# Kernel tuning notes

Hardware: AMD Instinct MI355X
Metric: run time of the kernel (lower is better)

Reference implementation:

```python
import jax, jax.numpy as jnp
import numpy as np

E, C, M, H, O = 8, 4096, 1024, 4096, 1024  # experts, capacity, model_dim, hidden, output_dim

def setup_inputs() -> dict:
    key = jax.random.key(0)
    k1, k2, k3, k4, k5 = jax.random.split(key, 5)
    s1 = 1.0 / np.sqrt(M)
    s2 = 1.0 / np.sqrt(H)
    return {
        "x": jax.random.normal(k1, (E, C, M), dtype=jnp.float32),
        "fc1_w": jax.random.normal(k2, (E, M, H), dtype=jnp.float32) * s1,
        "fc1_b": jax.random.normal(k3, (E, H), dtype=jnp.float32) * s1,
        "fc2_w": jax.random.normal(k4, (E, H, O), dtype=jnp.float32) * s2,
        "fc2_b": jax.random.normal(k5, (E, O), dtype=jnp.float32) * s2,
    }

def reference(x, fc1_w, fc1_b, fc2_w, fc2_b):
    # grouped GEMM over experts: [E,C,M] @ [E,M,H] -> [E,C,H]
    y = jnp.einsum('ecm,emh->ech', x, fc1_w) + fc1_b[:, None, :]
    y = jax.nn.relu(y)  # default activation_fn
    # [E,C,H] @ [E,H,O] -> [E,C,O]
    out = jnp.einsum('ech,eho->eco', y, fc2_w) + fc2_b[:, None, :]
    return out
```

## Files before the change

### kernel.cpp

```cpp
#include <hip/hip_runtime.h>
#include <hip/hip_bf16.h>


#define BM 128
#define BN 128
#define BK 32

typedef __attribute__((ext_vector_type(8))) short short8;
typedef __attribute__((ext_vector_type(4))) float f32x4;

typedef const __attribute__((address_space(1))) void GV;
typedef __attribute__((address_space(3))) void LV;

__device__ inline ushort f2bf_rne(float f) {
    union { float f; unsigned u; } v; v.f = f;
    unsigned u = v.u;
    u += 0x7FFFu + ((u >> 16) & 1u);
    return (ushort)(u >> 16);
}

__global__ __launch_bounds__(256) void convert_bf16(
    const float* __restrict__ in, ushort* __restrict__ out, long n) {
    long i = ((long)blockIdx.x * 256 + threadIdx.x) * 8;
    if (i + 7 >= n) return;
    float4 v0 = *(const float4*)&in[i];
    float4 v1 = *(const float4*)&in[i + 4];
    short8 o;
    o[0] = f2bf_rne(v0.x); o[1] = f2bf_rne(v0.y);
    o[2] = f2bf_rne(v0.z); o[3] = f2bf_rne(v0.w);
    o[4] = f2bf_rne(v1.x); o[5] = f2bf_rne(v1.y);
    o[6] = f2bf_rne(v1.z); o[7] = f2bf_rne(v1.w);
    *(short8*)&out[i] = o;
}

__global__ __launch_bounds__(256) void transpose_convert(
    const float* __restrict__ in, ushort* __restrict__ out, int R, int Cn) {
    __shared__ float tile[64][65];
    const int e  = blockIdx.z;
    const float* ine  = in  + (size_t)e * R * Cn;
    ushort*      oute = out + (size_t)e * R * Cn;
    const int r0 = blockIdx.y * 64;
    const int c0 = blockIdx.x * 64;
    const int t  = threadIdx.x;
#pragma unroll
    for (int i = 0; i < 4; ++i) {
        int idx = i * 256 + t;
        int ir  = idx >> 4;
        int icc = (idx & 15) * 4;
        float4 v = *(const float4*)&ine[(size_t)(r0 + ir) * Cn + c0 + icc];
        tile[ir][icc + 0] = v.x; tile[ir][icc + 1] = v.y;
        tile[ir][icc + 2] = v.z; tile[ir][icc + 3] = v.w;
    }
    __syncthreads();
#pragma unroll
    for (int i = 0; i < 2; ++i) {
        int idx = i * 256 + t;
        int ic  = idx >> 3;
        int ir0 = (idx & 7) * 8;
        short8 o;
#pragma unroll
        for (int j = 0; j < 8; ++j) o[j] = f2bf_rne(tile[ir0 + j][ic]);
        *(short8*)&oute[(size_t)(c0 + ic) * R + r0 + ir0] = o;
    }
}

template <bool RELU_BF16_OUT, int GX, int GY, int K, int N>
__global__ __launch_bounds__(256, 2) void gemm_bt(
    const ushort* __restrict__ A, const ushort* __restrict__ Bt,
    const float* __restrict__ bias, void* __restrict__ out) {
    __shared__ ushort As[BM * BK];
    __shared__ ushort Bs[BN * BK];

    constexpr int TOTAL   = GX * GY * 8;
    constexpr int ST_PER_E = (GY / 8) * (GX / 8);
    constexpr int ST_PER_X = TOTAL / 8 / 64;

    const int pid   = blockIdx.x;
    const int xcd   = pid & 7;
    const int local = pid >> 3;
    const int st    = xcd * ST_PER_X + (local >> 6);
    const int within = local & 63;
    const int e   = st / ST_PER_E;
    const int str = st % ST_PER_E;
    const int stm = str / (GX / 8);
    const int stn = str % (GX / 8);
    const int by  = stm * 8 + (within & 7);
    const int bx  = stn * 8 + (within >> 3);

    const int Crows = 4096;
    const ushort* Ae = A  + (size_t)e * Crows * K;
    const ushort* Be = Bt + (size_t)e * N * K;
    const float*  be = bias + (size_t)e * N;

    const int m0 = by * BM;
    const int n0 = bx * BN;

    const int t    = threadIdx.x;
    const int lane = t & 63;
    const int wave = t >> 6;
    const int wm   = (wave >> 1) * 64;
    const int wn   = (wave & 1) * 64;
    const int quad = lane >> 4;
    const int lrow = lane & 15;

    const int i0 = t, i1 = t + 256;
    const ushort* gA0 = Ae + (size_t)(m0 + (i0 >> 2)) * K + (i0 & 3) * 8;
    const ushort* gA1 = Ae + (size_t)(m0 + (i1 >> 2)) * K + (i1 & 3) * 8;
    const ushort* gB0 = Be + (size_t)(n0 + (i0 >> 2)) * K + (i0 & 3) * 8;
    const ushort* gB1 = Be + (size_t)(n0 + (i1 >> 2)) * K + (i1 & 3) * 8;
    ushort* lA0 = &As[i0 * 8];
    ushort* lA1 = &As[i1 * 8];
    ushort* lB0 = &Bs[i0 * 8];
    ushort* lB1 = &Bs[i1 * 8];

    f32x4 acc[4][4] = {};

    for (int k0 = 0; k0 < K; k0 += BK) {
        __builtin_amdgcn_global_load_lds((GV*)gA0, (LV*)lA0, 16, 0, 0);
        __builtin_amdgcn_global_load_lds((GV*)gA1, (LV*)lA1, 16, 0, 0);
        __builtin_amdgcn_global_load_lds((GV*)gB0, (LV*)lB0, 16, 0, 0);
        __builtin_amdgcn_global_load_lds((GV*)gB1, (LV*)lB1, 16, 0, 0);
        gA0 += BK; gA1 += BK; gB0 += BK; gB1 += BK;
        __syncthreads();

        short8 a[4], b[4];
#pragma unroll
        for (int i = 0; i < 4; ++i) {
            a[i] = *(const short8*)&As[(wm + i * 16 + lrow) * BK + quad * 8];
            b[i] = *(const short8*)&Bs[(wn + i * 16 + lrow) * BK + quad * 8];
        }
#pragma unroll
        for (int mi = 0; mi < 4; ++mi)
#pragma unroll
            for (int ni = 0; ni < 4; ++ni)
                acc[mi][ni] = __builtin_amdgcn_mfma_f32_16x16x32_bf16(
                    a[mi], b[ni], acc[mi][ni], 0, 0, 0);
        __syncthreads();
    }

#pragma unroll
    for (int mi = 0; mi < 4; ++mi) {
#pragma unroll
        for (int ni = 0; ni < 4; ++ni) {
            const int gn = n0 + wn + ni * 16 + lrow;
            const float bv = be[gn];
#pragma unroll
            for (int r = 0; r < 4; ++r) {
                const int gm = m0 + wm + mi * 16 + quad * 4 + r;
                float v = acc[mi][ni][r] + bv;
                if (RELU_BF16_OUT) {
                    v = fmaxf(v, 0.f);
                    ((ushort*)out)[(size_t)e * Crows * N + (size_t)gm * N + gn] =
                        f2bf_rne(v);
                } else {
                    ((float*)out)[(size_t)e * Crows * N + (size_t)gm * N + gn] = v;
                }
            }
        }
    }
}

extern "C" void kernel_launch(void* const* d_in, const int* in_sizes, int n_in,
                              void* d_out, int out_size, void* d_ws, size_t ws_size,
                              hipStream_t stream) {
    const int E = 8, C = 4096, M = 1024, H = 4096, O = 1024;
    const float* x  = (const float*)d_in[0];
    const float* w1 = (const float*)d_in[1];
    const float* b1 = (const float*)d_in[2];
    const float* w2 = (const float*)d_in[3];
    const float* b2 = (const float*)d_in[4];
    float* out = (float*)d_out;

    ushort* x_bf = (ushort*)d_ws;
    ushort* w1t  = x_bf + (size_t)E * C * M;
    ushort* w2t  = w1t;
    ushort* y_bf = w1t + (size_t)E * M * H;

    const long nx = (long)E * C * M;
    convert_bf16<<<(nx / 8 + 255) / 256, 256, 0, stream>>>(x, x_bf, nx);
    transpose_convert<<<dim3(H / 64, M / 64, E), 256, 0, stream>>>(w1, w1t, M, H);
    gemm_bt<true, 32, 32, 1024, 4096><<<32 * 32 * 8, 256, 0, stream>>>(
        x_bf, w1t, b1, (void*)y_bf);
    transpose_convert<<<dim3(O / 64, H / 64, E), 256, 0, stream>>>(w2, w2t, H, O);
    gemm_bt<false, 8, 32, 4096, 1024><<<8 * 32 * 8, 256, 0, stream>>>(
        y_bf, w2t, b2, (void*)out);
}
```

Before: 1.036 ms.

## Replace GEMM with 256x256 double-buffered 8-wave kernel using swizzled LDS

Replaces the 128x128x32 single-buffer GEMM with a 256x256x64 tile kernel of 8 waves that double-buffers LDS. Global-to-LDS loads for the next K tiles are interleaved with four MFMA quadrants per iteration, with raised wave priority around the MFMA blocks. An XOR swizzle on LDS columns avoids bank conflicts, and the block-to-tile mapping now groups blocks by expert. The goal is to hide memory latency and raise arithmetic intensity. The cost is much heavier LDS use (128KB per block) and register pressure, plus hand-written vmcnt and barrier choreography that is fragile.

Result: faster. 903.4 us (-12.8%).

```diff
diff --git a/kernel.cpp b/kernel.cpp
--- a/kernel.cpp
+++ b/kernel.cpp
@@ -2,15 +2,18 @@
 #include <hip/hip_bf16.h>
 
 
-#define BM 128
-#define BN 128
-#define BK 32
-
 typedef __attribute__((ext_vector_type(8))) short short8;
 typedef __attribute__((ext_vector_type(4))) float f32x4;
 
 typedef const __attribute__((address_space(1))) void GV;
 typedef __attribute__((address_space(3))) void LV;
+
+#define BAR()                                                                  \
+    do {                                                                       \
+        asm volatile("" ::: "memory");                                         \
+        __builtin_amdgcn_s_barrier();                                          \
+        asm volatile("" ::: "memory");                                         \
+    } while (0)
 
 __device__ inline ushort f2bf_rne(float f) {
     union { float f; unsigned u; } v; v.f = f;
@@ -64,96 +67,169 @@
     }
 }
 
-template <bool RELU_BF16_OUT, int GX, int GY, int K, int N>
-__global__ __launch_bounds__(256, 2) void gemm_bt(
+
+#define MFMA_Q(QM, QN)                                                         \
+    do {                                                                       \
+        _Pragma("unroll")                                                      \
+        for (int kh = 0; kh < 2; ++kh)                                         \
+            _Pragma("unroll")                                                  \
+            for (int mf = 0; mf < 4; ++mf)                                     \
+                _Pragma("unroll")                                              \
+                for (int nf = 0; nf < 2; ++nf)                                 \
+                    acc[(QM) * 4 + mf][(QN) * 2 + nf] =                        \
+                        __builtin_amdgcn_mfma_f32_16x16x32_bf16(               \
+                            a[(QM) * 4 + mf][kh], b[nf][kh],                   \
+                            acc[(QM) * 4 + mf][(QN) * 2 + nf], 0, 0, 0);       \
+    } while (0)
+
+#define STAGE(P0, P1_, HOFF, LBASE, TG)                                        \
+    do {                                                                       \
+        const int _tg = (TG);                                                  \
+        if (_tg < NTt) {                                                       \
+            const size_t _k = (size_t)_tg * 64;                                \
+            __builtin_amdgcn_global_load_lds((GV*)((P0) + (HOFF) + _k),        \
+                (LV*)&smem[(LBASE) + d0], 16, 0, 0);                           \
+            __builtin_amdgcn_global_load_lds((GV*)((P1_) + (HOFF) + _k),       \
+                (LV*)&smem[(LBASE) + d1], 16, 0, 0);                           \
+        }                                                                      \
+    } while (0)
+
+template <bool RELU_BF16_OUT, int MT, int NTILES, int K, int N>
+__global__ __launch_bounds__(512, 2) void gemm8p(
     const ushort* __restrict__ A, const ushort* __restrict__ Bt,
     const float* __restrict__ bias, void* __restrict__ out) {
-    __shared__ ushort As[BM * BK];
-    __shared__ ushort Bs[BN * BK];
-
-    constexpr int TOTAL   = GX * GY * 8;
-    constexpr int ST_PER_E = (GY / 8) * (GX / 8);
-    constexpr int ST_PER_X = TOTAL / 8 / 64;
-
-    const int pid   = blockIdx.x;
-    const int xcd   = pid & 7;
-    const int local = pid >> 3;
-    const int st    = xcd * ST_PER_X + (local >> 6);
-    const int within = local & 63;
-    const int e   = st / ST_PER_E;
-    const int str = st % ST_PER_E;
-    const int stm = str / (GX / 8);
-    const int stn = str % (GX / 8);
-    const int by  = stm * 8 + (within & 7);
-    const int bx  = stn * 8 + (within >> 3);
-
-    const int Crows = 4096;
-    const ushort* Ae = A  + (size_t)e * Crows * K;
+    __shared__ ushort smem[65536];
+    constexpr int NTt = K / 64;
+    constexpr int STC = NTILES / 4;
+
+    const int pid = blockIdx.x;
+    const int e   = pid & 7;
+    const int idx = pid >> 3;
+    const int s  = idx >> 4, wi = idx & 15;
+    const int by = (s / STC) * 4 + (wi >> 2);
+    const int bx = (s % STC) * 4 + (wi & 3);
+    const int m0 = by * 256, n0 = bx * 256;
+
+    const ushort* Ae = A  + (size_t)e * 4096 * K;
     const ushort* Be = Bt + (size_t)e * N * K;
     const float*  be = bias + (size_t)e * N;
 
-    const int m0 = by * BM;
-    const int n0 = bx * BN;
-
     const int t    = threadIdx.x;
-    const int lane = t & 63;
-    const int wave = t >> 6;
-    const int wm   = (wave >> 1) * 64;
-    const int wn   = (wave & 1) * 64;
-    const int quad = lane >> 4;
-    const int lrow = lane & 15;
-
-    const int i0 = t, i1 = t + 256;
-    const ushort* gA0 = Ae + (size_t)(m0 + (i0 >> 2)) * K + (i0 & 3) * 8;
-    const ushort* gA1 = Ae + (size_t)(m0 + (i1 >> 2)) * K + (i1 & 3) * 8;
-    const ushort* gB0 = Be + (size_t)(n0 + (i0 >> 2)) * K + (i0 & 3) * 8;
-    const ushort* gB1 = Be + (size_t)(n0 + (i1 >> 2)) * K + (i1 & 3) * 8;
-    ushort* lA0 = &As[i0 * 8];
-    ushort* lA1 = &As[i1 * 8];
-    ushort* lB0 = &Bs[i0 * 8];
-    ushort* lB1 = &Bs[i1 * 8];
-
-    f32x4 acc[4][4] = {};
-
-    for (int k0 = 0; k0 < K; k0 += BK) {
-        __builtin_amdgcn_global_load_lds((GV*)gA0, (LV*)lA0, 16, 0, 0);
-        __builtin_amdgcn_global_load_lds((GV*)gA1, (LV*)lA1, 16, 0, 0);
-        __builtin_amdgcn_global_load_lds((GV*)gB0, (LV*)lB0, 16, 0, 0);
-        __builtin_amdgcn_global_load_lds((GV*)gB1, (LV*)lB1, 16, 0, 0);
-        gA0 += BK; gA1 += BK; gB0 += BK; gB1 += BK;
-        __syncthreads();
-
-        short8 a[4], b[4];
-#pragma unroll
-        for (int i = 0; i < 4; ++i) {
-            a[i] = *(const short8*)&As[(wm + i * 16 + lrow) * BK + quad * 8];
-            b[i] = *(const short8*)&Bs[(wn + i * 16 + lrow) * BK + quad * 8];
+    const int w    = t >> 6, l = t & 63;
+    const int wm   = w >> 2;
+    const int wn   = w & 3;
+    const int lrow = l & 15, q = l >> 4;
+    const int swz  = (lrow & 7) << 3;
+
+    const int r0s = w * 16 + (l >> 3);
+    const int r1s = r0s + 8;
+    const int c0s = ((l & 7) ^ (r0s & 7)) << 3;
+    const int c1s = ((l & 7) ^ (r1s & 7)) << 3;
+    const int d0  = w * 1024 + l * 8;
+    const int d1  = d0 + 512;
+
+    const ushort* pa0 = Ae + (size_t)(m0 + r0s) * K + c0s;
+    const ushort* pa1 = Ae + (size_t)(m0 + r1s) * K + c1s;
+    const ushort* pb0 = Be + (size_t)(n0 + r0s) * K + c0s;
+    const ushort* pb1 = Be + (size_t)(n0 + r1s) * K + c1s;
+
+    float bv[4];
+#pragma unroll
+    for (int nf = 0; nf < 4; ++nf) bv[nf] = be[n0 + wn * 64 + nf * 16 + lrow];
+    asm volatile("s_waitcnt vmcnt(0)" ::: "memory");
+
+    STAGE(pa0, pa1, (size_t)0,       0,             0);
+    STAGE(pa0, pa1, (size_t)128 * K, 8192,          0);
+    STAGE(pb0, pb1, (size_t)0,       16384,         0);
+    STAGE(pb0, pb1, (size_t)128 * K, 16384 + 8192,  0);
+    STAGE(pa0, pa1, (size_t)0,       32768,         1);
+    STAGE(pa0, pa1, (size_t)128 * K, 32768 + 8192,  1);
+    asm volatile("s_waitcnt vmcnt(4)" ::: "memory");
+    BAR();
+
+    short8 a[8][2], b[2][2];
+    f32x4 acc[8][4] = {};
+
+    for (int ti = 0; ti < NTt; ++ti) {
+        const int buf  = ti & 1;
+        const int obuf = buf ^ 1;
+        const ushort* Ab = &smem[buf * 32768 + wm * 8192];
+        const ushort* Bb = &smem[buf * 32768 + 16384 + (wn >> 1) * 8192 +
+                                 (wn & 1) * 4096];
+
+#pragma unroll
+        for (int mf = 0; mf < 4; ++mf)
+#pragma unroll
+            for (int kh = 0; kh < 2; ++kh)
+                a[mf][kh] = *(const short8*)
+                    &Ab[(mf * 16 + lrow) * 64 + ((kh * 32 + q * 8) ^ swz)];
+#pragma unroll
+        for (int nf = 0; nf < 2; ++nf)
+#pragma unroll
+            for (int kh = 0; kh < 2; ++kh)
+                b[nf][kh] = *(const short8*)
+                    &Bb[(nf * 16 + lrow) * 64 + ((kh * 32 + q * 8) ^ swz)];
+        STAGE(pb0, pb1, (size_t)0, obuf * 32768 + 16384, ti + 1);
+        BAR();
+        __builtin_amdgcn_s_setprio(1);
+        MFMA_Q(0, 0);
+        __builtin_amdgcn_s_setprio(0);
+        BAR();
+
+#pragma unroll
+        for (int mf = 0; mf < 4; ++mf)
+#pragma unroll
+            for (int kh = 0; kh < 2; ++kh)
+                a[4 + mf][kh] = *(const short8*)
+                    &Ab[((4 + mf) * 16 + lrow) * 64 + ((kh * 32 + q * 8) ^ swz)];
+        STAGE(pb0, pb1, (size_t)128 * K, obuf * 32768 + 16384 + 8192, ti + 1);
+        BAR();
+        __builtin_amdgcn_s_setprio(1);
+        MFMA_Q(1, 0);
+        __builtin_amdgcn_s_setprio(0);
+        BAR();
+
+#pragma unroll
+        for (int nf = 0; nf < 2; ++nf)
+#pragma unroll
+            for (int kh = 0; kh < 2; ++kh)
+                b[nf][kh] = *(const short8*)
+                    &Bb[((2 + nf) * 16 + lrow) * 64 + ((kh * 32 + q * 8) ^ swz)];
+        STAGE(pa0, pa1, (size_t)0, buf * 32768, ti + 2);
+        BAR();
+        __builtin_amdgcn_s_setprio(1);
+        MFMA_Q(1, 1);
+        __builtin_amdgcn_s_setprio(0);
+        BAR();
+
+        STAGE(pa0, pa1, (size_t)128 * K, buf * 32768 + 8192, ti + 2);
+        BAR();
+        __builtin_amdgcn_s_setprio(1);
+        MFMA_Q(0, 1);
+        __builtin_amdgcn_s_setprio(0);
+        if (ti < NTt - 2) {
+            asm volatile("s_waitcnt vmcnt(4)" ::: "memory");
+        } else if (ti == NTt - 2) {
+            asm volatile("s_waitcnt vmcnt(0)" ::: "memory");
         }
-#pragma unroll
-        for (int mi = 0; mi < 4; ++mi)
-#pragma unroll
-            for (int ni = 0; ni < 4; ++ni)
-                acc[mi][ni] = __builtin_amdgcn_mfma_f32_16x16x32_bf16(
-                    a[mi], b[ni], acc[mi][ni], 0, 0, 0);
-        __syncthreads();
-    }
-
-#pragma unroll
-    for (int mi = 0; mi < 4; ++mi) {
-#pragma unroll
-        for (int ni = 0; ni < 4; ++ni) {
-            const int gn = n0 + wn + ni * 16 + lrow;
-            const float bv = be[gn];
-#pragma unroll
-            for (int r = 0; r < 4; ++r) {
-                const int gm = m0 + wm + mi * 16 + quad * 4 + r;
-                float v = acc[mi][ni][r] + bv;
+        BAR();
+    }
+
+    const size_t obase = (size_t)e * 4096 * N;
+#pragma unroll
+    for (int mf = 0; mf < 8; ++mf) {
+#pragma unroll
+        for (int nf = 0; nf < 4; ++nf) {
+            const int gn = n0 + wn * 64 + nf * 16 + lrow;
+#pragma unroll
+            for (int rr = 0; rr < 4; ++rr) {
+                const int gm = m0 + wm * 128 + mf * 16 + q * 4 + rr;
+                float v = acc[mf][nf][rr] + bv[nf];
                 if (RELU_BF16_OUT) {
                     v = fmaxf(v, 0.f);
-                    ((ushort*)out)[(size_t)e * Crows * N + (size_t)gm * N + gn] =
-                        f2bf_rne(v);
+                    ((ushort*)out)[obase + (size_t)gm * N + gn] = f2bf_rne(v);
                 } else {
-                    ((float*)out)[(size_t)e * Crows * N + (size_t)gm * N + gn] = v;
+                    ((float*)out)[obase + (size_t)gm * N + gn] = v;
                 }
             }
         }
@@ -179,9 +255,9 @@
     const long nx = (long)E * C * M;
     convert_bf16<<<(nx / 8 + 255) / 256, 256, 0, stream>>>(x, x_bf, nx);
     transpose_convert<<<dim3(H / 64, M / 64, E), 256, 0, stream>>>(w1, w1t, M, H);
-    gemm_bt<true, 32, 32, 1024, 4096><<<32 * 32 * 8, 256, 0, stream>>>(
+    gemm8p<true, 16, 16, 1024, 4096><<<16 * 16 * 8, 512, 0, stream>>>(
         x_bf, w1t, b1, (void*)y_bf);
     transpose_convert<<<dim3(O / 64, H / 64, E), 256, 0, stream>>>(w2, w2t, H, O);
-    gemm_bt<false, 8, 32, 4096, 1024><<<8 * 32 * 8, 256, 0, stream>>>(
+    gemm8p<false, 16, 4, 4096, 1024><<<16 * 4 * 8, 512, 0, stream>>>(
         y_bf, w2t, b2, (void*)out);
 }
```
